# Kernel optimization log

Measured on AMD Instinct MI355X. Metric: run time of the kernel, lower is better.

The kernel has to match this reference:

```python
import jax, jax.numpy as jnp
import numpy as np

NUM_EXPERTS = 8
NUM_TASKS = 2
NUM_INPUTS = 512
H_EXPERT = 256
H_TOWER = 64
BATCH = 16384


def setup_inputs() -> dict:
    key = jax.random.key(0)
    ks = jax.random.split(key, 7)
    s_in = 1.0 / np.sqrt(NUM_INPUTS)
    s_h = 1.0 / np.sqrt(H_EXPERT)
    return {
        "xv": jax.random.normal(ks[0], (BATCH, NUM_INPUTS), dtype=jnp.float32),
        # stacked expert Linear(num_inputs -> h_expert)
        "We": jax.random.uniform(ks[1], (NUM_EXPERTS, NUM_INPUTS, H_EXPERT), jnp.float32, -s_in, s_in),
        "be": jax.random.uniform(ks[2], (NUM_EXPERTS, H_EXPERT), jnp.float32, -s_in, s_in),
        # stacked gate Linear(num_inputs -> num_experts)
        "Wg": jax.random.uniform(ks[3], (NUM_TASKS, NUM_INPUTS, NUM_EXPERTS), jnp.float32, -s_in, s_in),
        "bg": jax.random.uniform(ks[4], (NUM_TASKS, NUM_EXPERTS), jnp.float32, -s_in, s_in),
        # stacked tower Linear(h_expert -> h_tower)
        "Wt": jax.random.uniform(ks[5], (NUM_TASKS, H_EXPERT, H_TOWER), jnp.float32, -s_h, s_h),
        "bt": jax.random.uniform(ks[6], (NUM_TASKS, H_TOWER), jnp.float32, -s_h, s_h),
    }


def reference(xv, We, be, Wg, bg, Wt, bt):
    # Experts: relu(x @ We_e + be_e)  -> [E, B, H]  (dropout is identity in eval)
    experts = jax.nn.relu(jnp.einsum('bi,eih->ebh', xv, We) + be[:, None, :])
    # Gates: softmax over experts -> [T, B, E]
    gates = jax.nn.softmax(jnp.einsum('bi,tie->tbe', xv, Wg) + bg[:, None, :], axis=-1)
    # Weighted mixture per task -> [T, B, H]
    tower_in = jnp.einsum('tbe,ebh->tbh', gates, experts)
    # Towers + sigmoid -> [T, B, O]
    out = jax.nn.sigmoid(jnp.einsum('tbh,tho->tbo', tower_in, Wt) + bt[:, None, :])
    return (out[0], out[1])
```

## Files before the change

kernel.cpp:

```cpp
#include <hip/hip_runtime.h>
#include <hip/hip_bf16.h>

#define B_   16384
#define KIN  512
#define NE   8
#define HE   256
#define NT   2
#define NO   64

using f32x4  = __attribute__((ext_vector_type(4))) float;
using short8 = __attribute__((ext_vector_type(8))) short;

typedef const __attribute__((address_space(1))) void* gas_ptr;
typedef __attribute__((address_space(3))) void* las_ptr;

__device__ __forceinline__ float bf2f(unsigned short u) {
    union { unsigned int i; float f; } c; c.i = ((unsigned int)u) << 16; return c.f;
}
__device__ __forceinline__ unsigned short f2bf(float f) {
    union { __hip_bfloat16 h; unsigned short u; } c; c.h = __float2bfloat16(f); return c.u;
}

__global__ __launch_bounds__(256) void k_cvt_w(const float* __restrict__ We,
                                               const float* __restrict__ Wt,
                                               const float* __restrict__ Wg,
                                               unsigned short* __restrict__ Wb,
                                               unsigned short* __restrict__ WtT,
                                               unsigned short* __restrict__ WgT) {
    int bid = blockIdx.x;
    int tid = threadIdx.x;
    if (bid < 256) {
        __shared__ float tile[64][65];
        int e = bid >> 5, rem = bid & 31, kt = rem >> 2, ht = rem & 3;
        const float* src = We + e * (KIN * HE) + (kt * 64) * HE + ht * 64;
        for (int it = 0; it < 16; ++it) {
            int idx = tid + it * 256;
            int i = idx >> 6, j = idx & 63;
            tile[i][j] = src[i * HE + j];
        }
        __syncthreads();
        unsigned short* dst = Wb + (size_t)(e * HE + ht * 64) * KIN + kt * 64;
        for (int it = 0; it < 16; ++it) {
            int idx = tid + it * 256;
            int i = idx >> 6, j = idx & 63;
            dst[i * KIN + j] = f2bf(tile[j][i]);
        }
    } else if (bid < 264) {
        __shared__ float tile[64][65];
        int b = bid - 256;
        int t = b >> 2, kt = b & 3, k0 = kt * 64;
        const float* src = Wt + t * (HE * NO) + k0 * NO;
        for (int it = 0; it < 16; ++it) {
            int idx = tid + it * 256;
            int i = idx >> 6, j = idx & 63;
            tile[i][j] = src[i * NO + j];
        }
        __syncthreads();
        unsigned short* dst = WtT + (size_t)t * NO * HE + k0;
        for (int it = 0; it < 16; ++it) {
            int idx = tid + it * 256;
            int o = idx >> 6, j = idx & 63;
            dst[o * HE + j] = f2bf(tile[j][o]);
        }
    } else {
        int n = tid >> 4;
        int kb = (tid & 15) * 32;
        int t = n >> 3, e = n & 7;
        const float* src = Wg + t * (KIN * NE) + e;
        for (int j = 0; j < 32; ++j) {
            int k = kb + j;
            WgT[n * KIN + k] = f2bf(src[k * NE]);
        }
    }
}

__global__ __launch_bounds__(512, 2) void k_mega(const float* __restrict__ xv,
                                                 const unsigned short* __restrict__ Wb,
                                                 const float* __restrict__ be,
                                                 const unsigned short* __restrict__ WgT,
                                                 const float* __restrict__ bg,
                                                 const unsigned short* __restrict__ WtT,
                                                 const float* __restrict__ bt,
                                                 float* __restrict__ out) {
    __shared__ __align__(16) char smem[135424];
    unsigned short* Xs  = (unsigned short*)smem;
    unsigned short* Bs  = (unsigned short*)(smem + 65536);
    float*          gs  = (float*)(smem + 131072);
    unsigned short* TIs = (unsigned short*)smem;

    int tid = threadIdx.x, lane = tid & 63, wav = tid >> 6;
    int l15 = lane & 15, l4 = lane >> 4;
    int swz = (l15 & 7) * 8;
    int wv32 = wav * 32;
    int r0 = blockIdx.x * 64;

    int row_off = lane >> 3;
    int sco = ((lane & 7) ^ row_off) * 8;

    auto stage_b = [&](int s) {
        int e = s >> 3, kt = s & 7, b = s & 1;
        const unsigned short* Wbase = Wb + (size_t)(e * 256 + wv32) * KIN + kt * 64;
        #pragma unroll
        for (int i = 0; i < 4; ++i) {
            int rb = i * 8;
            __builtin_amdgcn_global_load_lds(
                (gas_ptr)(Wbase + (size_t)(rb + row_off) * KIN + sco),
                (las_ptr)(Bs + b * 16384 + (wv32 + rb) * 64), 16, 0, 0);
        }
    };

    #pragma unroll
    for (int j = 0; j < 8; ++j) {
        int row = wav * 8 + j;
        const float4* src = (const float4*)(xv + (size_t)(r0 + row) * KIN) + lane * 2;
        float4 xa = src[0], xb = src[1];
        union { short8 v; unsigned short s[8]; } cv;
        cv.s[0] = f2bf(xa.x); cv.s[1] = f2bf(xa.y); cv.s[2] = f2bf(xa.z); cv.s[3] = f2bf(xa.w);
        cv.s[4] = f2bf(xb.x); cv.s[5] = f2bf(xb.y); cv.s[6] = f2bf(xb.z); cv.s[7] = f2bf(xb.w);
        *(short8*)(Xs + row * KIN + ((lane ^ (row & 7)) * 8)) = cv.v;
    }
    asm volatile("s_waitcnt lgkmcnt(0)" ::: "memory");
    asm volatile("s_barrier" ::: "memory");

    stage_b(0);

    {
        int m0w = (wav & 3) * 16;
        f32x4 ga = {0.f, 0.f, 0.f, 0.f};
        #pragma unroll
        for (int kk = 0; kk < 16; ++kk) {
            short8 a = *(const short8*)(Xs + (m0w + l15) * KIN + ((kk * 32 + l4 * 8) ^ swz));
            short8 b = *(const short8*)(WgT + (size_t)l15 * KIN + kk * 32 + l4 * 8);
            ga = __builtin_amdgcn_mfma_f32_16x16x32_bf16(a, b, ga, 0, 0, 0);
        }
        float bias = bg[l15];
        #pragma unroll
        for (int r = 0; r < 4; ++r) {
            float v = ga[r] + bias;
            float m = v;
            m = fmaxf(m, __shfl_xor(m, 1));
            m = fmaxf(m, __shfl_xor(m, 2));
            m = fmaxf(m, __shfl_xor(m, 4));
            float p = __expf(v - m);
            float su = p;
            su += __shfl_xor(su, 1);
            su += __shfl_xor(su, 2);
            su += __shfl_xor(su, 4);
            gs[(m0w + l4 * 4 + r) * 17 + l15] = p / su;
        }
    }
    asm volatile("s_waitcnt lgkmcnt(0)" ::: "memory");
    asm volatile("s_barrier" ::: "memory");

    f32x4 acc[4][2];
    f32x4 ti0[4][2], ti1[4][2];
    f32x4 z = {0.f, 0.f, 0.f, 0.f};
    #pragma unroll
    for (int mf = 0; mf < 4; ++mf)
        #pragma unroll
        for (int nf = 0; nf < 2; ++nf) { acc[mf][nf] = z; ti0[mf][nf] = z; ti1[mf][nf] = z; }

    auto compute = [&](int s) {
        int k0 = (s & 7) * 64, b = s & 1;
        __builtin_amdgcn_s_setprio(1);
        #pragma unroll
        for (int kk = 0; kk < 2; ++kk) {
            short8 a[4], bb[2];
            int kca = (k0 + kk * 32 + l4 * 8) ^ swz;
            int kcb = (kk * 32 + l4 * 8) ^ swz;
            #pragma unroll
            for (int mf = 0; mf < 4; ++mf)
                a[mf] = *(const short8*)(Xs + (mf * 16 + l15) * KIN + kca);
            #pragma unroll
            for (int nf = 0; nf < 2; ++nf)
                bb[nf] = *(const short8*)(Bs + b * 16384 + (wv32 + nf * 16 + l15) * 64 + kcb);
            #pragma unroll
            for (int mf = 0; mf < 4; ++mf)
                #pragma unroll
                for (int nf = 0; nf < 2; ++nf)
                    acc[mf][nf] = __builtin_amdgcn_mfma_f32_16x16x32_bf16(a[mf], bb[nf], acc[mf][nf], 0, 0, 0);
        }
        __builtin_amdgcn_s_setprio(0);
    };
    auto fold = [&](int e) {
        float b0 = be[e * 256 + wv32 + l15];
        float b1 = be[e * 256 + wv32 + 16 + l15];
        #pragma unroll
        for (int mf = 0; mf < 4; ++mf) {
            #pragma unroll
            for (int r = 0; r < 4; ++r) {
                int rloc = mf * 16 + l4 * 4 + r;
                float g0 = gs[rloc * 17 + e];
                float g1 = gs[rloc * 17 + 8 + e];
                float h0 = fmaxf(acc[mf][0][r] + b0, 0.f);
                float h1 = fmaxf(acc[mf][1][r] + b1, 0.f);
                ti0[mf][0][r] = fmaf(g0, h0, ti0[mf][0][r]);
                ti0[mf][1][r] = fmaf(g0, h1, ti0[mf][1][r]);
                ti1[mf][0][r] = fmaf(g1, h0, ti1[mf][0][r]);
                ti1[mf][1][r] = fmaf(g1, h1, ti1[mf][1][r]);
                acc[mf][0][r] = 0.f;
                acc[mf][1][r] = 0.f;
            }
        }
    };

    #pragma unroll 8
    for (int s = 0; s < 64; ++s) {
        if (s < 63) {
            stage_b(s + 1);
            asm volatile("s_waitcnt vmcnt(4)" ::: "memory");
        } else {
            asm volatile("s_waitcnt vmcnt(0)" ::: "memory");
        }
        compute(s);
        if ((s & 7) == 7) fold(s >> 3);
    }

    __syncthreads();
    #pragma unroll
    for (int mf = 0; mf < 4; ++mf)
        #pragma unroll
        for (int nf = 0; nf < 2; ++nf)
            #pragma unroll
            for (int r = 0; r < 4; ++r) {
                int row = mf * 16 + l4 * 4 + r;
                int col = wv32 + nf * 16 + l15;
                TIs[(0 * 64 + row) * 264 + col] = f2bf(ti0[mf][nf][r]);
                TIs[(1 * 64 + row) * 264 + col] = f2bf(ti1[mf][nf][r]);
            }
    __syncthreads();

    {
        int tt = wav >> 2, m0t = (wav & 3) * 16;
        f32x4 ac[4];
        #pragma unroll
        for (int nf = 0; nf < 4; ++nf) ac[nf] = z;
        #pragma unroll
        for (int kk = 0; kk < 8; ++kk) {
            int kcol = kk * 32 + l4 * 8;
            short8 a = *(const short8*)(TIs + ((size_t)(tt * 64 + m0t + l15)) * 264 + kcol);
            #pragma unroll
            for (int nf = 0; nf < 4; ++nf) {
                short8 b = *(const short8*)(WtT + ((size_t)tt * NO + nf * 16 + l15) * HE + kcol);
                ac[nf] = __builtin_amdgcn_mfma_f32_16x16x32_bf16(a, b, ac[nf], 0, 0, 0);
            }
        }
        #pragma unroll
        for (int nf = 0; nf < 4; ++nf) {
            int col = nf * 16 + l15;
            float bias = bt[tt * NO + col];
            #pragma unroll
            for (int r = 0; r < 4; ++r) {
                int row = r0 + m0t + l4 * 4 + r;
                float v = ac[nf][r] + bias;
                v = 1.f / (1.f + __expf(-v));
                out[(size_t)tt * (B_ * NO) + (size_t)row * NO + col] = v;
            }
        }
    }
}

extern "C" void kernel_launch(void* const* d_in, const int* in_sizes, int n_in,
                              void* d_out, int out_size, void* d_ws, size_t ws_size,
                              hipStream_t stream) {
    const float* xv = (const float*)d_in[0];
    const float* We = (const float*)d_in[1];
    const float* be = (const float*)d_in[2];
    const float* Wg = (const float*)d_in[3];
    const float* bg = (const float*)d_in[4];
    const float* Wt = (const float*)d_in[5];
    const float* bt = (const float*)d_in[6];
    float* out = (float*)d_out;

    char* w = (char*)d_ws;
    unsigned short* Wb  = (unsigned short*)(w);
    unsigned short* WtT = (unsigned short*)(w + 2097152);
    unsigned short* WgT = (unsigned short*)(w + 2162688);

    k_cvt_w<<<265, 256, 0, stream>>>(We, Wt, Wg, Wb, WtT, WgT);
    k_mega<<<256, 512, 0, stream>>>(xv, Wb, be, WgT, bg, WtT, bt, out);
}
```

Baseline: 62.02 us.

## Pre-swizzle expert weights into MFMA fragment order and load directly to registers

The weight conversion kernel now writes expert weights in per-wave, per-lane MFMA B-fragment order. The main kernel can then fetch each B operand with one coalesced 16-byte global load straight into registers, double-buffered one step ahead. This removes the LDS staging buffer for B, its async global-to-LDS copies and the LDS reads, and halves the shared memory footprint. In exchange, global load latency is hidden only by a one-stage register prefetch without explicit waitcnt control, and register pressure rises.

```diff
diff --git a/kernel.cpp b/kernel.cpp
--- a/kernel.cpp
+++ b/kernel.cpp
@@ -11,9 +11,6 @@
 using f32x4  = __attribute__((ext_vector_type(4))) float;
 using short8 = __attribute__((ext_vector_type(8))) short;
 
-typedef const __attribute__((address_space(1))) void* gas_ptr;
-typedef __attribute__((address_space(3))) void* las_ptr;
-
 __device__ __forceinline__ float bf2f(unsigned short u) {
     union { unsigned int i; float f; } c; c.i = ((unsigned int)u) << 16; return c.f;
 }
@@ -24,7 +21,7 @@
 __global__ __launch_bounds__(256) void k_cvt_w(const float* __restrict__ We,
                                                const float* __restrict__ Wt,
                                                const float* __restrict__ Wg,
-                                               unsigned short* __restrict__ Wb,
+                                               unsigned short* __restrict__ Wb2,
                                                unsigned short* __restrict__ WtT,
                                                unsigned short* __restrict__ WgT) {
     int bid = blockIdx.x;
@@ -39,11 +36,16 @@
             tile[i][j] = src[i * HE + j];
         }
         __syncthreads();
-        unsigned short* dst = Wb + (size_t)(e * HE + ht * 64) * KIN + kt * 64;
-        for (int it = 0; it < 16; ++it) {
-            int idx = tid + it * 256;
-            int i = idx >> 6, j = idx & 63;
-            dst[i * KIN + j] = f2bf(tile[j][i]);
+        int s = e * 8 + kt;
+        for (int it = 0; it < 16; ++it) {
+            int o = tid + it * 256;
+            int j = o & 7, lane = (o >> 3) & 63;
+            int nf = (o >> 9) & 1, wavl = (o >> 10) & 1, kk = (o >> 11) & 1;
+            int l4 = lane >> 4, l15 = lane & 15;
+            int ksub = kk * 32 + l4 * 8 + j;
+            int hsub = wavl * 32 + nf * 16 + l15;
+            size_t F = ((((size_t)(s * 2 + kk) * 8 + (ht * 2 + wavl)) * 2 + nf) * 64 + lane) * 8 + j;
+            Wb2[F] = f2bf(tile[ksub][hsub]);
         }
     } else if (bid < 264) {
         __shared__ float tile[64][65];
@@ -75,17 +77,16 @@
 }
 
 __global__ __launch_bounds__(512, 2) void k_mega(const float* __restrict__ xv,
-                                                 const unsigned short* __restrict__ Wb,
+                                                 const unsigned short* __restrict__ Wb2,
                                                  const float* __restrict__ be,
                                                  const unsigned short* __restrict__ WgT,
                                                  const float* __restrict__ bg,
                                                  const unsigned short* __restrict__ WtT,
                                                  const float* __restrict__ bt,
                                                  float* __restrict__ out) {
-    __shared__ __align__(16) char smem[135424];
+    __shared__ __align__(16) char smem[69888];
     unsigned short* Xs  = (unsigned short*)smem;
-    unsigned short* Bs  = (unsigned short*)(smem + 65536);
-    float*          gs  = (float*)(smem + 131072);
+    float*          gs  = (float*)(smem + 65536);
     unsigned short* TIs = (unsigned short*)smem;
 
     int tid = threadIdx.x, lane = tid & 63, wav = tid >> 6;
@@ -93,21 +94,6 @@
     int swz = (l15 & 7) * 8;
     int wv32 = wav * 32;
     int r0 = blockIdx.x * 64;
-
-    int row_off = lane >> 3;
-    int sco = ((lane & 7) ^ row_off) * 8;
-
-    auto stage_b = [&](int s) {
-        int e = s >> 3, kt = s & 7, b = s & 1;
-        const unsigned short* Wbase = Wb + (size_t)(e * 256 + wv32) * KIN + kt * 64;
-        #pragma unroll
-        for (int i = 0; i < 4; ++i) {
-            int rb = i * 8;
-            __builtin_amdgcn_global_load_lds(
-                (gas_ptr)(Wbase + (size_t)(rb + row_off) * KIN + sco),
-                (las_ptr)(Bs + b * 16384 + (wv32 + rb) * 64), 16, 0, 0);
-        }
-    };
 
     #pragma unroll
     for (int j = 0; j < 8; ++j) {
@@ -119,10 +105,7 @@
         cv.s[4] = f2bf(xb.x); cv.s[5] = f2bf(xb.y); cv.s[6] = f2bf(xb.z); cv.s[7] = f2bf(xb.w);
         *(short8*)(Xs + row * KIN + ((lane ^ (row & 7)) * 8)) = cv.v;
     }
-    asm volatile("s_waitcnt lgkmcnt(0)" ::: "memory");
-    asm volatile("s_barrier" ::: "memory");
-
-    stage_b(0);
+    __syncthreads();
 
     {
         int m0w = (wav & 3) * 16;
@@ -149,8 +132,7 @@
             gs[(m0w + l4 * 4 + r) * 17 + l15] = p / su;
         }
     }
-    asm volatile("s_waitcnt lgkmcnt(0)" ::: "memory");
-    asm volatile("s_barrier" ::: "memory");
+    __syncthreads();
 
     f32x4 acc[4][2];
     f32x4 ti0[4][2], ti1[4][2];
@@ -160,27 +142,14 @@
         #pragma unroll
         for (int nf = 0; nf < 2; ++nf) { acc[mf][nf] = z; ti0[mf][nf] = z; ti1[mf][nf] = z; }
 
-    auto compute = [&](int s) {
-        int k0 = (s & 7) * 64, b = s & 1;
-        __builtin_amdgcn_s_setprio(1);
-        #pragma unroll
-        for (int kk = 0; kk < 2; ++kk) {
-            short8 a[4], bb[2];
-            int kca = (k0 + kk * 32 + l4 * 8) ^ swz;
-            int kcb = (kk * 32 + l4 * 8) ^ swz;
-            #pragma unroll
-            for (int mf = 0; mf < 4; ++mf)
-                a[mf] = *(const short8*)(Xs + (mf * 16 + l15) * KIN + kca);
+    short8 pb[2][2], nb[2][2];
+    auto loadB = [&](int s, short8 (&d)[2][2]) {
+        #pragma unroll
+        for (int kk = 0; kk < 2; ++kk)
             #pragma unroll
             for (int nf = 0; nf < 2; ++nf)
-                bb[nf] = *(const short8*)(Bs + b * 16384 + (wv32 + nf * 16 + l15) * 64 + kcb);
-            #pragma unroll
-            for (int mf = 0; mf < 4; ++mf)
-                #pragma unroll
-                for (int nf = 0; nf < 2; ++nf)
-                    acc[mf][nf] = __builtin_amdgcn_mfma_f32_16x16x32_bf16(a[mf], bb[nf], acc[mf][nf], 0, 0, 0);
-        }
-        __builtin_amdgcn_s_setprio(0);
+                d[kk][nf] = *(const short8*)(Wb2 +
+                    ((((size_t)(s * 2 + kk) * 8 + wav) * 2 + nf) << 9) + lane * 8);
     };
     auto fold = [&](int e) {
         float b0 = be[e * 256 + wv32 + l15];
@@ -204,16 +173,32 @@
         }
     };
 
+    loadB(0, pb);
     #pragma unroll 8
     for (int s = 0; s < 64; ++s) {
-        if (s < 63) {
-            stage_b(s + 1);
-            asm volatile("s_waitcnt vmcnt(4)" ::: "memory");
-        } else {
-            asm volatile("s_waitcnt vmcnt(0)" ::: "memory");
-        }
-        compute(s);
+        if (s < 63) loadB(s + 1, nb);
+        int k0 = (s & 7) * 64;
+        __builtin_amdgcn_s_setprio(1);
+        #pragma unroll
+        for (int kk = 0; kk < 2; ++kk) {
+            short8 a[4];
+            int kca = (k0 + kk * 32 + l4 * 8) ^ swz;
+            #pragma unroll
+            for (int mf = 0; mf < 4; ++mf)
+                a[mf] = *(const short8*)(Xs + (mf * 16 + l15) * KIN + kca);
+            #pragma unroll
+            for (int mf = 0; mf < 4; ++mf)
+                #pragma unroll
+                for (int nf = 0; nf < 2; ++nf)
+                    acc[mf][nf] = __builtin_amdgcn_mfma_f32_16x16x32_bf16(a[mf], pb[kk][nf], acc[mf][nf], 0, 0, 0);
+        }
+        __builtin_amdgcn_s_setprio(0);
         if ((s & 7) == 7) fold(s >> 3);
+        #pragma unroll
+        for (int kk = 0; kk < 2; ++kk)
+            #pragma unroll
+            for (int nf = 0; nf < 2; ++nf)
+                pb[kk][nf] = nb[kk][nf];
     }
 
     __syncthreads();
@@ -273,10 +258,10 @@
     float* out = (float*)d_out;
 
     char* w = (char*)d_ws;
-    unsigned short* Wb  = (unsigned short*)(w);
+    unsigned short* Wb2 = (unsigned short*)(w);
     unsigned short* WtT = (unsigned short*)(w + 2097152);
     unsigned short* WgT = (unsigned short*)(w + 2162688);
 
-    k_cvt_w<<<265, 256, 0, stream>>>(We, Wt, Wg, Wb, WtT, WgT);
-    k_mega<<<256, 512, 0, stream>>>(xv, Wb, be, WgT, bg, WtT, bt, out);
-}
+    k_cvt_w<<<265, 256, 0, stream>>>(We, Wt, Wg, Wb2, WtT, WgT);
+    k_mega<<<256, 512, 0, stream>>>(xv, Wb2, be, WgT, bg, WtT, bt, out);
+}
```

New measurement: 151.2 us. +143.8%, slower.

## Interleave expert pairs so X fragments from LDS are reused across two experts

Applied to the files above, without the earlier changes.

Reorders the 64-stage loop so consecutive stages alternate between two experts at the same K tile. The A (X) fragments are loaded from LDS once and reused for both experts, and two accumulator sets are kept, folded together every 16 stages. The aim is to halve LDS reads of X per MFMA. In exchange, accumulator and A-fragment register use roughly doubles, which can raise VGPR pressure and lower occupancy.

```diff
diff --git a/kernel.cpp b/kernel.cpp
--- a/kernel.cpp
+++ b/kernel.cpp
@@ -98,7 +98,8 @@
     int sco = ((lane & 7) ^ row_off) * 8;
 
     auto stage_b = [&](int s) {
-        int e = s >> 3, kt = s & 7, b = s & 1;
+        int ep = s >> 4, kt = (s >> 1) & 7, ei = s & 1;
+        int e = ep * 2 + ei, b = s & 1;
         const unsigned short* Wbase = Wb + (size_t)(e * 256 + wv32) * KIN + kt * 64;
         #pragma unroll
         for (int i = 0; i < 4; ++i) {
@@ -152,37 +153,18 @@
     asm volatile("s_waitcnt lgkmcnt(0)" ::: "memory");
     asm volatile("s_barrier" ::: "memory");
 
-    f32x4 acc[4][2];
+    f32x4 acc[2][4][2];
     f32x4 ti0[4][2], ti1[4][2];
     f32x4 z = {0.f, 0.f, 0.f, 0.f};
     #pragma unroll
     for (int mf = 0; mf < 4; ++mf)
         #pragma unroll
-        for (int nf = 0; nf < 2; ++nf) { acc[mf][nf] = z; ti0[mf][nf] = z; ti1[mf][nf] = z; }
-
-    auto compute = [&](int s) {
-        int k0 = (s & 7) * 64, b = s & 1;
-        __builtin_amdgcn_s_setprio(1);
-        #pragma unroll
-        for (int kk = 0; kk < 2; ++kk) {
-            short8 a[4], bb[2];
-            int kca = (k0 + kk * 32 + l4 * 8) ^ swz;
-            int kcb = (kk * 32 + l4 * 8) ^ swz;
-            #pragma unroll
-            for (int mf = 0; mf < 4; ++mf)
-                a[mf] = *(const short8*)(Xs + (mf * 16 + l15) * KIN + kca);
-            #pragma unroll
-            for (int nf = 0; nf < 2; ++nf)
-                bb[nf] = *(const short8*)(Bs + b * 16384 + (wv32 + nf * 16 + l15) * 64 + kcb);
-            #pragma unroll
-            for (int mf = 0; mf < 4; ++mf)
-                #pragma unroll
-                for (int nf = 0; nf < 2; ++nf)
-                    acc[mf][nf] = __builtin_amdgcn_mfma_f32_16x16x32_bf16(a[mf], bb[nf], acc[mf][nf], 0, 0, 0);
-        }
-        __builtin_amdgcn_s_setprio(0);
-    };
-    auto fold = [&](int e) {
+        for (int nf = 0; nf < 2; ++nf) {
+            acc[0][mf][nf] = z; acc[1][mf][nf] = z;
+            ti0[mf][nf] = z; ti1[mf][nf] = z;
+        }
+
+    auto fold = [&](int e, f32x4 (&ac)[4][2]) {
         float b0 = be[e * 256 + wv32 + l15];
         float b1 = be[e * 256 + wv32 + 16 + l15];
         #pragma unroll
@@ -192,19 +174,20 @@
                 int rloc = mf * 16 + l4 * 4 + r;
                 float g0 = gs[rloc * 17 + e];
                 float g1 = gs[rloc * 17 + 8 + e];
-                float h0 = fmaxf(acc[mf][0][r] + b0, 0.f);
-                float h1 = fmaxf(acc[mf][1][r] + b1, 0.f);
+                float h0 = fmaxf(ac[mf][0][r] + b0, 0.f);
+                float h1 = fmaxf(ac[mf][1][r] + b1, 0.f);
                 ti0[mf][0][r] = fmaf(g0, h0, ti0[mf][0][r]);
                 ti0[mf][1][r] = fmaf(g0, h1, ti0[mf][1][r]);
                 ti1[mf][0][r] = fmaf(g1, h0, ti1[mf][0][r]);
                 ti1[mf][1][r] = fmaf(g1, h1, ti1[mf][1][r]);
-                acc[mf][0][r] = 0.f;
-                acc[mf][1][r] = 0.f;
+                ac[mf][0][r] = 0.f;
+                ac[mf][1][r] = 0.f;
             }
         }
     };
 
-    #pragma unroll 8
+    short8 a2[2][4];
+    #pragma unroll 16
     for (int s = 0; s < 64; ++s) {
         if (s < 63) {
             stage_b(s + 1);
@@ -212,8 +195,35 @@
         } else {
             asm volatile("s_waitcnt vmcnt(0)" ::: "memory");
         }
-        compute(s);
-        if ((s & 7) == 7) fold(s >> 3);
+        int kt = (s >> 1) & 7, ei = s & 1, b = s & 1;
+        int k0 = kt * 64;
+        __builtin_amdgcn_s_setprio(1);
+        #pragma unroll
+        for (int kk = 0; kk < 2; ++kk) {
+            if (ei == 0) {
+                int kca = (k0 + kk * 32 + l4 * 8) ^ swz;
+                #pragma unroll
+                for (int mf = 0; mf < 4; ++mf)
+                    a2[kk][mf] = *(const short8*)(Xs + (mf * 16 + l15) * KIN + kca);
+            }
+            short8 bb[2];
+            int kcb = (kk * 32 + l4 * 8) ^ swz;
+            #pragma unroll
+            for (int nf = 0; nf < 2; ++nf)
+                bb[nf] = *(const short8*)(Bs + b * 16384 + (wv32 + nf * 16 + l15) * 64 + kcb);
+            #pragma unroll
+            for (int mf = 0; mf < 4; ++mf)
+                #pragma unroll
+                for (int nf = 0; nf < 2; ++nf)
+                    acc[ei][mf][nf] = __builtin_amdgcn_mfma_f32_16x16x32_bf16(
+                        a2[kk][mf], bb[nf], acc[ei][mf][nf], 0, 0, 0);
+        }
+        __builtin_amdgcn_s_setprio(0);
+        if ((s & 15) == 15) {
+            int ep = s >> 4;
+            fold(ep * 2, acc[0]);
+            fold(ep * 2 + 1, acc[1]);
+        }
     }
 
     __syncthreads();
```

After: 246.4 us. +297.3%, slower.
